# Optimization experiments

Hardware: AMD Instinct MI355X
Metric: run time of the kernel (lower is better)

## Reference

```python
import jax, jax.numpy as jnp
import numpy as np

HEADS = 16
DIM_HEAD = 64
QUERY_DIM = 1024
CONTEXT_DIM = 1024
INNER = HEADS * DIM_HEAD  # 1024


def setup_inputs() -> dict:
    key = jax.random.key(0)
    k1, k2, k3, k4, k5, k6, k7 = jax.random.split(key, 7)
    B, N, M = 4, 2048, 2048
    s = 0.02
    return {
        "x": jax.random.normal(k1, (B, N, QUERY_DIM), jnp.float32),
        "context": jax.random.normal(k2, (B, M, CONTEXT_DIM), jnp.float32),
        "Wq": jax.random.normal(k3, (INNER, QUERY_DIM), jnp.float32) * s,
        "Wk": jax.random.normal(k4, (INNER, CONTEXT_DIM), jnp.float32) * s,
        "Wv": jax.random.normal(k5, (INNER, CONTEXT_DIM), jnp.float32) * s,
        "Wo": jax.random.normal(k6, (QUERY_DIM, INNER), jnp.float32) * s,
        "bo": jax.random.normal(k7, (QUERY_DIM,), jnp.float32) * s,
    }


def reference(x, context, Wq, Wk, Wv, Wo, bo):
    B, N, _ = x.shape
    M = context.shape[1]
    scale = DIM_HEAD ** (-0.5)
    # projections (torch Linear: y = x @ W.T)
    q = jnp.einsum('bnd,ed->bne', x, Wq)
    k = jnp.einsum('bmd,ed->bme', context, Wk)
    v = jnp.einsum('bmd,ed->bme', context, Wv)
    # split heads: b n (h d) -> b h n d
    q = q.reshape(B, N, HEADS, DIM_HEAD).transpose(0, 2, 1, 3)
    k = k.reshape(B, M, HEADS, DIM_HEAD).transpose(0, 2, 1, 3)
    v = v.reshape(B, M, HEADS, DIM_HEAD).transpose(0, 2, 1, 3)
    sim = jnp.einsum('bhid,bhjd->bhij', q, k) * scale
    attn = jax.nn.softmax(sim, axis=-1)
    out = jnp.einsum('bhij,bhjd->bhid', attn, v)
    out = out.transpose(0, 2, 1, 3).reshape(B, N, INNER)
    return jnp.einsum('bne,oe->bno', out, Wo) + bo
```

## Files before the change

kernel.cpp:

```cpp
#include <hip/hip_runtime.h>
#include <hip/hip_bf16.h>
#include <stdint.h>

#define HEADS 16
#define DIMH  64
#define SEQN  2048
#define SEQM  2048
#define NB    4
#define EDIM  1024
#define KD    1024

using bf16_t = __bf16;
using bf16x8 = __attribute__((ext_vector_type(8))) bf16_t;
using f32x4  = __attribute__((ext_vector_type(4))) float;

__device__ __forceinline__ unsigned short f2bf(float f) {
  union { float f; uint32_t u; } v; v.f = f;
  uint32_t u = v.u;
  u += 0x7fffu + ((u >> 16) & 1u);
  return (unsigned short)(u >> 16);
}

#if __has_builtin(__builtin_amdgcn_cvt_pk_bf16_f32)
typedef __bf16 bf16x2_t __attribute__((ext_vector_type(2)));
__device__ __forceinline__ uint32_t pk_bf16(float a, float b) {
  union { bf16x2_t v; uint32_t u; } c;
  c.v = __builtin_amdgcn_cvt_pk_bf16_f32(a, b);
  return c.u;
}
#else
__device__ __forceinline__ uint32_t pk_bf16(float a, float b) {
  union { __hip_bfloat162 v; uint32_t u; } c;
  c.v = __float22bfloat162_rn(float2{a, b});
  return c.u;
}
#endif

#if __has_builtin(__builtin_amdgcn_exp2f)
__device__ __forceinline__ float fexp2(float x) { return __builtin_amdgcn_exp2f(x); }
#else
__device__ __forceinline__ float fexp2(float x) { return exp2f(x); }
#endif

__device__ __forceinline__ void async16(const void* g, void* l) {
  __builtin_amdgcn_global_load_lds(
      (__attribute__((address_space(1))) void*)(g),
      (__attribute__((address_space(3))) void*)(l), 16, 0, 0);
}

__device__ __forceinline__ bf16x8 ldsv(const unsigned short* p) {
  return *(const bf16x8*)p;
}

__global__ __launch_bounds__(256)
void cvt2(const float4* __restrict__ a, const float4* __restrict__ b,
          ushort4* __restrict__ oa, ushort4* __restrict__ ob, int blocks_per_seg) {
  const int seg = blockIdx.x / blocks_per_seg;
  const int i = (blockIdx.x - seg * blocks_per_seg) * 256 + threadIdx.x;
  const float4* in = seg ? b : a;
  ushort4* out = seg ? ob : oa;
  float4 v = in[i];
  ushort4 o;
  o.x = f2bf(v.x); o.y = f2bf(v.y); o.z = f2bf(v.z); o.w = f2bf(v.w);
  out[i] = o;
}

__global__ __launch_bounds__(256)
void cvt4(const float4* __restrict__ a, const float4* __restrict__ b,
          const float4* __restrict__ c, const float4* __restrict__ d,
          ushort4* __restrict__ oa, ushort4* __restrict__ ob,
          ushort4* __restrict__ oc, ushort4* __restrict__ od, int blocks_per_seg) {
  const int seg = blockIdx.x / blocks_per_seg;
  const int i = (blockIdx.x - seg * blocks_per_seg) * 256 + threadIdx.x;
  const float4* in = (seg == 0) ? a : (seg == 1) ? b : (seg == 2) ? c : d;
  ushort4* out = (seg == 0) ? oa : (seg == 1) ? ob : (seg == 2) ? oc : od;
  float4 v = in[i];
  ushort4 o;
  o.x = f2bf(v.x); o.y = f2bf(v.y); o.z = f2bf(v.z); o.w = f2bf(v.w);
  out[i] = o;
}

__global__ __launch_bounds__(256)
void gemm_qkv(const unsigned short* __restrict__ xb,
              const unsigned short* __restrict__ cb,
              const unsigned short* __restrict__ wqb,
              const unsigned short* __restrict__ wkb,
              const unsigned short* __restrict__ wvb,
              unsigned short* __restrict__ Qb,
              unsigned short* __restrict__ Kb,
              unsigned short* __restrict__ Vtb,
              float qscale)
{
  __shared__ __align__(16) unsigned short As[128 * 32];
  __shared__ __align__(16) unsigned short Bs[128 * 32];
  const int t   = threadIdx.x;
  const int wv  = t >> 6;
  const int ln  = t & 63;
  const int l15 = ln & 15;
  const int qd  = ln >> 4;

  const int L   = blockIdx.x;
  const int xcd = L & 7;
  const int n0  = ((L >> 3) & 7) * 128;
  const int mq  = (L >> 6) & 7;
  const int z   = L >> 9;
  const int m0  = (mq * 8 + xcd) * 128;

  const int wm  = (wv >> 1) * 64;
  const int wn  = (wv & 1) * 64;

  const unsigned short* A = (z == 0) ? xb : cb;
  const unsigned short* W = (z == 0) ? wqb : (z == 1) ? wkb : wvb;

  const f32x4 vzero = {0.f, 0.f, 0.f, 0.f};
  f32x4 acc[4][4];
#pragma unroll
  for (int i = 0; i < 4; ++i)
#pragma unroll
    for (int j = 0; j < 4; ++j) acc[i][j] = vzero;

  for (int k0 = 0; k0 < KD; k0 += 32) {
    __syncthreads();
#pragma unroll
    for (int l = 0; l < 2; ++l) {
      const int i = l * 256 + wv * 64 + ln;
      const int row = i >> 2, ch = i & 3;
      async16(A + (size_t)(m0 + row) * KD + k0 + ch * 8, As + i * 8);
      async16(W + (size_t)(n0 + row) * KD + k0 + ch * 8, Bs + i * 8);
    }
    __syncthreads();
    bf16x8 af[4], bfr[4];
#pragma unroll
    for (int mt = 0; mt < 4; ++mt)
      af[mt] = ldsv(As + (wm + mt * 16 + l15) * 32 + qd * 8);
#pragma unroll
    for (int nt = 0; nt < 4; ++nt)
      bfr[nt] = ldsv(Bs + (wn + nt * 16 + l15) * 32 + qd * 8);
#pragma unroll
    for (int mt = 0; mt < 4; ++mt)
#pragma unroll
      for (int nt = 0; nt < 4; ++nt)
        acc[mt][nt] = __builtin_amdgcn_mfma_f32_16x16x32_bf16(af[mt], bfr[nt], acc[mt][nt], 0, 0, 0);
  }

  const float scale = (z == 0) ? qscale : 1.0f;
#pragma unroll
  for (int mt = 0; mt < 4; ++mt) {
#pragma unroll
    for (int nt = 0; nt < 4; ++nt) {
      const int col   = n0 + wn + nt * 16 + l15;
      const int rbase = m0 + wm + mt * 16 + qd * 4;
      if (z < 2) {
        unsigned short* outb = (z == 0) ? Qb : Kb;
#pragma unroll
        for (int r = 0; r < 4; ++r)
          outb[(size_t)(rbase + r) * EDIM + col] = f2bf(acc[mt][nt][r] * scale);
      } else {
        const int b = rbase >> 11, m = rbase & 2047;
        const int h = col >> 6,   d = col & 63;
        ushort4 o;
        o.x = f2bf(acc[mt][nt][0]); o.y = f2bf(acc[mt][nt][1]);
        o.z = f2bf(acc[mt][nt][2]); o.w = f2bf(acc[mt][nt][3]);
        *(ushort4*)(Vtb + ((size_t)(b * HEADS + h) * DIMH + d) * SEQM + m) = o;
      }
    }
  }
}

__global__ __launch_bounds__(256)
void gemm_out(const unsigned short* __restrict__ A,
              const unsigned short* __restrict__ W,
              float* __restrict__ outf,
              const float* __restrict__ bias)
{
  __shared__ __align__(16) unsigned short As[128 * 32];
  __shared__ __align__(16) unsigned short Bs[128 * 32];
  const int t   = threadIdx.x;
  const int wv  = t >> 6;
  const int ln  = t & 63;
  const int l15 = ln & 15;
  const int qd  = ln >> 4;

  const int L   = blockIdx.x;
  const int xcd = L & 7;
  const int n0  = ((L >> 3) & 7) * 128;
  const int mq  = L >> 6;
  const int m0  = (mq * 8 + xcd) * 128;

  const int wm  = (wv >> 1) * 64;
  const int wn  = (wv & 1) * 64;

  const f32x4 vzero = {0.f, 0.f, 0.f, 0.f};
  f32x4 acc[4][4];
#pragma unroll
  for (int i = 0; i < 4; ++i)
#pragma unroll
    for (int j = 0; j < 4; ++j) acc[i][j] = vzero;

  for (int k0 = 0; k0 < KD; k0 += 32) {
    __syncthreads();
#pragma unroll
    for (int l = 0; l < 2; ++l) {
      const int i = l * 256 + wv * 64 + ln;
      const int row = i >> 2, ch = i & 3;
      async16(A + (size_t)(m0 + row) * KD + k0 + ch * 8, As + i * 8);
      async16(W + (size_t)(n0 + row) * KD + k0 + ch * 8, Bs + i * 8);
    }
    __syncthreads();
    bf16x8 af[4], bfr[4];
#pragma unroll
    for (int mt = 0; mt < 4; ++mt)
      af[mt] = ldsv(As + (wm + mt * 16 + l15) * 32 + qd * 8);
#pragma unroll
    for (int nt = 0; nt < 4; ++nt)
      bfr[nt] = ldsv(Bs + (wn + nt * 16 + l15) * 32 + qd * 8);
#pragma unroll
    for (int mt = 0; mt < 4; ++mt)
#pragma unroll
      for (int nt = 0; nt < 4; ++nt)
        acc[mt][nt] = __builtin_amdgcn_mfma_f32_16x16x32_bf16(af[mt], bfr[nt], acc[mt][nt], 0, 0, 0);
  }

#pragma unroll
  for (int mt = 0; mt < 4; ++mt) {
#pragma unroll
    for (int nt = 0; nt < 4; ++nt) {
      const int col   = n0 + wn + nt * 16 + l15;
      const int rbase = m0 + wm + mt * 16 + qd * 4;
      const float bv = bias[col];
#pragma unroll
      for (int r = 0; r < 4; ++r)
        outf[(size_t)(rbase + r) * EDIM + col] = acc[mt][nt][r] + bv;
    }
  }
}

__global__ __launch_bounds__(256)
void attn_kernel(const unsigned short* __restrict__ Q,
                 const unsigned short* __restrict__ K,
                 const unsigned short* __restrict__ VT,
                 unsigned short* __restrict__ O)
{
  __shared__ __align__(16) unsigned short Qs[128 * 64];
  __shared__ __align__(16) unsigned short Ks[64 * 64];
  __shared__ __align__(16) unsigned short Vs[64 * 64];
  unsigned short* Ps = Qs;

  const int t   = threadIdx.x;
  const int wv  = t >> 6;
  const int ln  = t & 63;
  const int l15 = ln & 15;
  const int qd  = ln >> 4;

  const int L      = blockIdx.x;
  const int bh     = ((L >> 7) << 3) | (L & 7);
  const int qt     = (L >> 3) & 15;
  const int q0     = qt * 128;
  const int b      = bh >> 4;
  const int h      = bh & 15;

  const unsigned short* Qp = Q + (size_t)b * SEQN * EDIM + h * DIMH;
  const unsigned short* Kp = K + (size_t)b * SEQM * EDIM + h * DIMH;
  const unsigned short* Vp = VT + ((size_t)bh) * DIMH * SEQM;

#pragma unroll
  for (int l = 0; l < 4; ++l) {
    const int i = l * 256 + wv * 64 + ln;
    const int row = i >> 3, ch = i & 7;
    const int gch = ch ^ (row & 7);
    async16(Qp + (size_t)(q0 + row) * EDIM + gch * 8, Qs + i * 8);
  }
  __syncthreads();

  bf16x8 qf[2][2];
#pragma unroll
  for (int qc = 0; qc < 2; ++qc) {
    const int row = wv * 32 + qc * 16 + l15;
#pragma unroll
    for (int ks = 0; ks < 2; ++ks) {
      const int c = (ks * 4 + qd) ^ (row & 7);
      qf[qc][ks] = ldsv(Qs + row * 64 + c * 8);
    }
  }

  const f32x4 vzero = {0.f, 0.f, 0.f, 0.f};
  f32x4 o_acc[2][4];
#pragma unroll
  for (int qc = 0; qc < 2; ++qc)
#pragma unroll
    for (int dt = 0; dt < 4; ++dt) o_acc[qc][dt] = vzero;

  float rsum[2] = {0.f, 0.f};

  unsigned short* Pw = Ps + wv * 2048;

  for (int j0 = 0; j0 < SEQM; j0 += 64) {
    __syncthreads();
#pragma unroll
    for (int l = 0; l < 2; ++l) {
      const int i = l * 256 + wv * 64 + ln;
      const int row = i >> 3, ch = i & 7;
      const int gch = ch ^ (row & 7);
      async16(Kp + (size_t)(j0 + row) * EDIM + gch * 8, Ks + i * 8);
      async16(Vp + (size_t)row * SEQM + j0 + gch * 8, Vs + i * 8);
    }
    __syncthreads();

    f32x4 st[2][4];
#pragma unroll
    for (int qc = 0; qc < 2; ++qc)
#pragma unroll
      for (int jt = 0; jt < 4; ++jt) st[qc][jt] = vzero;

#pragma unroll
    for (int jt = 0; jt < 4; ++jt) {
      const int rowj = jt * 16 + l15;
#pragma unroll
      for (int ks = 0; ks < 2; ++ks) {
        const int c = (ks * 4 + qd) ^ (rowj & 7);
        const bf16x8 kf = ldsv(Ks + rowj * 64 + c * 8);
        st[0][jt] = __builtin_amdgcn_mfma_f32_16x16x32_bf16(kf, qf[0][ks], st[0][jt], 0, 0, 0);
        st[1][jt] = __builtin_amdgcn_mfma_f32_16x16x32_bf16(kf, qf[1][ks], st[1][jt], 0, 0, 0);
      }
    }

#pragma unroll
    for (int qc = 0; qc < 2; ++qc) {
      unsigned short* prow = Pw + (qc * 16 + l15) * 64;
#pragma unroll
      for (int jt = 0; jt < 4; ++jt) {
        float p0 = fexp2(st[qc][jt][0]);
        float p1 = fexp2(st[qc][jt][1]);
        float p2 = fexp2(st[qc][jt][2]);
        float p3 = fexp2(st[qc][jt][3]);
        rsum[qc] += (p0 + p1) + (p2 + p3);
        uint2 dw;
        dw.x = pk_bf16(p0, p1);
        dw.y = pk_bf16(p2, p3);
        const int c = (jt * 4 + qd) ^ l15;
        *(uint2*)(prow + c * 4) = dw;
      }
    }
    asm volatile("" ::: "memory");

#pragma unroll
    for (int ks2 = 0; ks2 < 2; ++ks2) {
      bf16x8 pf[2];
#pragma unroll
      for (int qc = 0; qc < 2; ++qc) {
        const unsigned short* prow = Pw + (qc * 16 + l15) * 64;
        const int c0 = ks2 * 8 + qd * 2;
        uint2 lo = *(const uint2*)(prow + ((c0)     ^ l15) * 4);
        uint2 hi = *(const uint2*)(prow + ((c0 + 1) ^ l15) * 4);
        union { uint32_t u[4]; bf16x8 v; } cc;
        cc.u[0] = lo.x; cc.u[1] = lo.y; cc.u[2] = hi.x; cc.u[3] = hi.y;
        pf[qc] = cc.v;
      }
#pragma unroll
      for (int dt = 0; dt < 4; ++dt) {
        const int rowd = dt * 16 + l15;
        const int c = (ks2 * 4 + qd) ^ (rowd & 7);
        const bf16x8 vf = ldsv(Vs + rowd * 64 + c * 8);
        o_acc[0][dt] = __builtin_amdgcn_mfma_f32_16x16x32_bf16(pf[0], vf, o_acc[0][dt], 0, 0, 0);
        o_acc[1][dt] = __builtin_amdgcn_mfma_f32_16x16x32_bf16(pf[1], vf, o_acc[1][dt], 0, 0, 0);
      }
    }
  }

#pragma unroll
  for (int qc = 0; qc < 2; ++qc) {
    float r = rsum[qc];
    r += __shfl_xor(r, 16);
    r += __shfl_xor(r, 32);
    rsum[qc] = r;
  }

  unsigned short* Op = O + (size_t)b * SEQN * EDIM + h * DIMH;
#pragma unroll
  for (int qc = 0; qc < 2; ++qc) {
    float inv[4];
#pragma unroll
    for (int r = 0; r < 4; ++r)
      inv[r] = 1.0f / __shfl(rsum[qc], qd * 4 + r);
#pragma unroll
    for (int dt = 0; dt < 4; ++dt) {
      const int col = dt * 16 + l15;
#pragma unroll
      for (int r = 0; r < 4; ++r) {
        const int row = q0 + wv * 32 + qc * 16 + qd * 4 + r;
        Op[(size_t)row * EDIM + col] = f2bf(o_acc[qc][dt][r] * inv[r]);
      }
    }
  }
}

extern "C" void kernel_launch(void* const* d_in, const int* in_sizes, int n_in,
                              void* d_out, int out_size, void* d_ws, size_t ws_size,
                              hipStream_t stream) {
  const float* x   = (const float*)d_in[0];
  const float* ctx = (const float*)d_in[1];
  const float* Wq  = (const float*)d_in[2];
  const float* Wk  = (const float*)d_in[3];
  const float* Wv  = (const float*)d_in[4];
  const float* Wo  = (const float*)d_in[5];
  const float* bo  = (const float*)d_in[6];
  float* out = (float*)d_out;

  char* ws = (char*)d_ws;
  const size_t SZ_X = (size_t)NB * SEQN * EDIM * 2;
  const size_t SZ_W = (size_t)EDIM * KD * 2;
  unsigned short* xb  = (unsigned short*)(ws);
  unsigned short* cb  = (unsigned short*)(ws + SZ_X);
  unsigned short* wqb = (unsigned short*)(ws + 2 * SZ_X);
  unsigned short* wkb = (unsigned short*)(ws + 2 * SZ_X + SZ_W);
  unsigned short* wvb = (unsigned short*)(ws + 2 * SZ_X + 2 * SZ_W);
  unsigned short* wob = (unsigned short*)(ws + 2 * SZ_X + 3 * SZ_W);
  unsigned short* Qb  = (unsigned short*)(ws + 2 * SZ_X + 4 * SZ_W);
  unsigned short* Kb  = (unsigned short*)(ws + 3 * SZ_X + 4 * SZ_W);
  unsigned short* Vtb = (unsigned short*)(ws + 4 * SZ_X + 4 * SZ_W);
  unsigned short* Ob  = (unsigned short*)(ws + 5 * SZ_X + 4 * SZ_W);

  const int n4x = (NB * SEQN * EDIM) / 4;
  const int n4w = (EDIM * KD) / 4;
  const int bpx = n4x / 256;
  const int bpw = n4w / 256;
  cvt2<<<2 * bpx, 256, 0, stream>>>((const float4*)x, (const float4*)ctx,
                                    (ushort4*)xb, (ushort4*)cb, bpx);
  cvt4<<<4 * bpw, 256, 0, stream>>>((const float4*)Wq, (const float4*)Wk,
                                    (const float4*)Wv, (const float4*)Wo,
                                    (ushort4*)wqb, (ushort4*)wkb,
                                    (ushort4*)wvb, (ushort4*)wob, bpw);

  const float SCL2E = 0.125f * 1.4426950408889634f;
  const dim3 blk(256);

  gemm_qkv<<<dim3(1536), blk, 0, stream>>>(
      xb, cb, wqb, wkb, wvb, Qb, Kb, Vtb, SCL2E);

  attn_kernel<<<dim3(1024), blk, 0, stream>>>(Qb, Kb, Vtb, Ob);

  gemm_out<<<dim3(512), blk, 0, stream>>>(Ob, wob, out, bo);
}
```

Baseline: 329.0 us.

## Double GEMM K-tile to 64 with XOR-swizzled LDS and merge conversion kernels

Both projection GEMMs now stage 64-wide K slices per iteration instead of 32, which halves the number of barrier pairs and load rounds. The LDS layout uses an XOR swizzle on the 16-byte chunks so the row-strided MFMA fragment reads avoid bank conflicts. The two fp32-to-bf16 conversion launches are merged into one kernel, saving a launch. In exchange, LDS use per block doubles, which may lower occupancy.

```diff
diff --git a/kernel.cpp b/kernel.cpp
--- a/kernel.cpp
+++ b/kernel.cpp
@@ -53,27 +53,21 @@
 }
 
 __global__ __launch_bounds__(256)
-void cvt2(const float4* __restrict__ a, const float4* __restrict__ b,
-          ushort4* __restrict__ oa, ushort4* __restrict__ ob, int blocks_per_seg) {
-  const int seg = blockIdx.x / blocks_per_seg;
-  const int i = (blockIdx.x - seg * blocks_per_seg) * 256 + threadIdx.x;
-  const float4* in = seg ? b : a;
-  ushort4* out = seg ? ob : oa;
-  float4 v = in[i];
-  ushort4 o;
-  o.x = f2bf(v.x); o.y = f2bf(v.y); o.z = f2bf(v.z); o.w = f2bf(v.w);
-  out[i] = o;
-}
-
-__global__ __launch_bounds__(256)
-void cvt4(const float4* __restrict__ a, const float4* __restrict__ b,
-          const float4* __restrict__ c, const float4* __restrict__ d,
-          ushort4* __restrict__ oa, ushort4* __restrict__ ob,
-          ushort4* __restrict__ oc, ushort4* __restrict__ od, int blocks_per_seg) {
-  const int seg = blockIdx.x / blocks_per_seg;
-  const int i = (blockIdx.x - seg * blocks_per_seg) * 256 + threadIdx.x;
-  const float4* in = (seg == 0) ? a : (seg == 1) ? b : (seg == 2) ? c : d;
-  ushort4* out = (seg == 0) ? oa : (seg == 1) ? ob : (seg == 2) ? oc : od;
+void cvt_all(const float4* __restrict__ x,  const float4* __restrict__ ctx,
+             const float4* __restrict__ wq, const float4* __restrict__ wk,
+             const float4* __restrict__ wv, const float4* __restrict__ wo,
+             ushort4* __restrict__ xb,  ushort4* __restrict__ cb,
+             ushort4* __restrict__ wqb, ushort4* __restrict__ wkb,
+             ushort4* __restrict__ wvb, ushort4* __restrict__ wob) {
+  const int bid = blockIdx.x;
+  const float4* in; ushort4* out; int i0;
+  if (bid < 8192)       { in = x;   out = xb;  i0 = bid; }
+  else if (bid < 16384) { in = ctx; out = cb;  i0 = bid - 8192; }
+  else if (bid < 17408) { in = wq;  out = wqb; i0 = bid - 16384; }
+  else if (bid < 18432) { in = wk;  out = wkb; i0 = bid - 17408; }
+  else if (bid < 19456) { in = wv;  out = wvb; i0 = bid - 18432; }
+  else                  { in = wo;  out = wob; i0 = bid - 19456; }
+  const int i = i0 * 256 + threadIdx.x;
   float4 v = in[i];
   ushort4 o;
   o.x = f2bf(v.x); o.y = f2bf(v.y); o.z = f2bf(v.z); o.w = f2bf(v.w);
@@ -91,8 +85,8 @@
               unsigned short* __restrict__ Vtb,
               float qscale)
 {
-  __shared__ __align__(16) unsigned short As[128 * 32];
-  __shared__ __align__(16) unsigned short Bs[128 * 32];
+  __shared__ __align__(16) unsigned short As[128 * 64];
+  __shared__ __align__(16) unsigned short Bs[128 * 64];
   const int t   = threadIdx.x;
   const int wv  = t >> 6;
   const int ln  = t & 63;
@@ -119,28 +113,36 @@
 #pragma unroll
     for (int j = 0; j < 4; ++j) acc[i][j] = vzero;
 
-  for (int k0 = 0; k0 < KD; k0 += 32) {
-    __syncthreads();
-#pragma unroll
-    for (int l = 0; l < 2; ++l) {
+  for (int k0 = 0; k0 < KD; k0 += 64) {
+    __syncthreads();
+#pragma unroll
+    for (int l = 0; l < 4; ++l) {
       const int i = l * 256 + wv * 64 + ln;
-      const int row = i >> 2, ch = i & 3;
-      async16(A + (size_t)(m0 + row) * KD + k0 + ch * 8, As + i * 8);
-      async16(W + (size_t)(n0 + row) * KD + k0 + ch * 8, Bs + i * 8);
-    }
-    __syncthreads();
-    bf16x8 af[4], bfr[4];
-#pragma unroll
-    for (int mt = 0; mt < 4; ++mt)
-      af[mt] = ldsv(As + (wm + mt * 16 + l15) * 32 + qd * 8);
-#pragma unroll
-    for (int nt = 0; nt < 4; ++nt)
-      bfr[nt] = ldsv(Bs + (wn + nt * 16 + l15) * 32 + qd * 8);
-#pragma unroll
-    for (int mt = 0; mt < 4; ++mt)
-#pragma unroll
-      for (int nt = 0; nt < 4; ++nt)
-        acc[mt][nt] = __builtin_amdgcn_mfma_f32_16x16x32_bf16(af[mt], bfr[nt], acc[mt][nt], 0, 0, 0);
+      const int row = i >> 3, ch = i & 7;
+      const int gch = ch ^ (row & 7);
+      async16(A + (size_t)(m0 + row) * KD + k0 + gch * 8, As + i * 8);
+      async16(W + (size_t)(n0 + row) * KD + k0 + gch * 8, Bs + i * 8);
+    }
+    __syncthreads();
+#pragma unroll
+    for (int ks = 0; ks < 2; ++ks) {
+      bf16x8 af[4], bfr[4];
+#pragma unroll
+      for (int mt = 0; mt < 4; ++mt) {
+        const int row = wm + mt * 16 + l15;
+        af[mt] = ldsv(As + row * 64 + (((ks * 4 + qd) ^ (row & 7)) * 8));
+      }
+#pragma unroll
+      for (int nt = 0; nt < 4; ++nt) {
+        const int row = wn + nt * 16 + l15;
+        bfr[nt] = ldsv(Bs + row * 64 + (((ks * 4 + qd) ^ (row & 7)) * 8));
+      }
+#pragma unroll
+      for (int mt = 0; mt < 4; ++mt)
+#pragma unroll
+        for (int nt = 0; nt < 4; ++nt)
+          acc[mt][nt] = __builtin_amdgcn_mfma_f32_16x16x32_bf16(af[mt], bfr[nt], acc[mt][nt], 0, 0, 0);
+    }
   }
 
   const float scale = (z == 0) ? qscale : 1.0f;
@@ -173,8 +175,8 @@
               float* __restrict__ outf,
               const float* __restrict__ bias)
 {
-  __shared__ __align__(16) unsigned short As[128 * 32];
-  __shared__ __align__(16) unsigned short Bs[128 * 32];
+  __shared__ __align__(16) unsigned short As[128 * 64];
+  __shared__ __align__(16) unsigned short Bs[128 * 64];
   const int t   = threadIdx.x;
   const int wv  = t >> 6;
   const int ln  = t & 63;
@@ -197,28 +199,36 @@
 #pragma unroll
     for (int j = 0; j < 4; ++j) acc[i][j] = vzero;
 
-  for (int k0 = 0; k0 < KD; k0 += 32) {
-    __syncthreads();
-#pragma unroll
-    for (int l = 0; l < 2; ++l) {
+  for (int k0 = 0; k0 < KD; k0 += 64) {
+    __syncthreads();
+#pragma unroll
+    for (int l = 0; l < 4; ++l) {
       const int i = l * 256 + wv * 64 + ln;
-      const int row = i >> 2, ch = i & 3;
-      async16(A + (size_t)(m0 + row) * KD + k0 + ch * 8, As + i * 8);
-      async16(W + (size_t)(n0 + row) * KD + k0 + ch * 8, Bs + i * 8);
-    }
-    __syncthreads();
-    bf16x8 af[4], bfr[4];
-#pragma unroll
-    for (int mt = 0; mt < 4; ++mt)
-      af[mt] = ldsv(As + (wm + mt * 16 + l15) * 32 + qd * 8);
-#pragma unroll
-    for (int nt = 0; nt < 4; ++nt)
-      bfr[nt] = ldsv(Bs + (wn + nt * 16 + l15) * 32 + qd * 8);
-#pragma unroll
-    for (int mt = 0; mt < 4; ++mt)
-#pragma unroll
-      for (int nt = 0; nt < 4; ++nt)
-        acc[mt][nt] = __builtin_amdgcn_mfma_f32_16x16x32_bf16(af[mt], bfr[nt], acc[mt][nt], 0, 0, 0);
+      const int row = i >> 3, ch = i & 7;
+      const int gch = ch ^ (row & 7);
+      async16(A + (size_t)(m0 + row) * KD + k0 + gch * 8, As + i * 8);
+      async16(W + (size_t)(n0 + row) * KD + k0 + gch * 8, Bs + i * 8);
+    }
+    __syncthreads();
+#pragma unroll
+    for (int ks = 0; ks < 2; ++ks) {
+      bf16x8 af[4], bfr[4];
+#pragma unroll
+      for (int mt = 0; mt < 4; ++mt) {
+        const int row = wm + mt * 16 + l15;
+        af[mt] = ldsv(As + row * 64 + (((ks * 4 + qd) ^ (row & 7)) * 8));
+      }
+#pragma unroll
+      for (int nt = 0; nt < 4; ++nt) {
+        const int row = wn + nt * 16 + l15;
+        bfr[nt] = ldsv(Bs + row * 64 + (((ks * 4 + qd) ^ (row & 7)) * 8));
+      }
+#pragma unroll
+      for (int mt = 0; mt < 4; ++mt)
+#pragma unroll
+        for (int nt = 0; nt < 4; ++nt)
+          acc[mt][nt] = __builtin_amdgcn_mfma_f32_16x16x32_bf16(af[mt], bfr[nt], acc[mt][nt], 0, 0, 0);
+    }
   }
 
 #pragma unroll
@@ -420,20 +430,15 @@
   unsigned short* Vtb = (unsigned short*)(ws + 4 * SZ_X + 4 * SZ_W);
   unsigned short* Ob  = (unsigned short*)(ws + 5 * SZ_X + 4 * SZ_W);
 
-  const int n4x = (NB * SEQN * EDIM) / 4;
-  const int n4w = (EDIM * KD) / 4;
-  const int bpx = n4x / 256;
-  const int bpw = n4w / 256;
-  cvt2<<<2 * bpx, 256, 0, stream>>>((const float4*)x, (const float4*)ctx,
-                                    (ushort4*)xb, (ushort4*)cb, bpx);
-  cvt4<<<4 * bpw, 256, 0, stream>>>((const float4*)Wq, (const float4*)Wk,
-                                    (const float4*)Wv, (const float4*)Wo,
-                                    (ushort4*)wqb, (ushort4*)wkb,
-                                    (ushort4*)wvb, (ushort4*)wob, bpw);
-
   const float SCL2E = 0.125f * 1.4426950408889634f;
   const dim3 blk(256);
 
+  cvt_all<<<dim3(20480), blk, 0, stream>>>(
+      (const float4*)x, (const float4*)ctx, (const float4*)Wq, (const float4*)Wk,
+      (const float4*)Wv, (const float4*)Wo,
+      (ushort4*)xb, (ushort4*)cb, (ushort4*)wqb, (ushort4*)wkb,
+      (ushort4*)wvb, (ushort4*)wob);
+
   gemm_qkv<<<dim3(1536), blk, 0, stream>>>(
       xb, cb, wqb, wkb, wvb, Qb, Kb, Vtb, SCL2E);
 
```

Result: faster. 315.5 us (-4.1%).
